# Kernel optimization log

Hardware: AMD Instinct MI355X
Metric: run time of the kernel (lower is better)

The kernel has to match this reference:

```python
import jax, jax.numpy as jnp
import numpy as np
import math

B, T, H = 2, 1024, 2048
NH, NKV, HD = 8, 2, 256
S = 4           # altup_num_inputs
FF = 8192       # intermediate_size
LR = 64         # laurel_rank
EPS = 1e-6
ROPE_THETA = 1e6


def _ln(x, w):
    # Gemma3nRMSNorm in this repo: fp32 mean-subtract then F.layer_norm (no bias)
    x32 = x.astype(jnp.float32)
    xc = x32 - x32.mean(-1, keepdims=True)
    var = (xc * xc).mean(-1, keepdims=True)
    return (xc * jax.lax.rsqrt(var + EPS) * w.astype(jnp.float32)).astype(x.dtype)


def _rotate_half(x):
    x1, x2 = jnp.split(x, 2, axis=-1)
    return jnp.concatenate((-x2, x1), axis=-1)


def _rope(x, cos, sin):  # x: [B,nh,T,hd]; cos/sin: [B,T,hd]
    return x * cos[:, None] + _rotate_half(x) * sin[:, None]


def setup_inputs() -> dict:
    key = jax.random.key(0)
    ks = jax.random.split(key, 24)

    def w(k, shape, scale=0.02):
        return jax.random.normal(k, shape, jnp.float32) * scale

    hidden_states = jax.random.normal(ks[0], (S, B, T, H), jnp.float32)

    # real rotary embeddings
    inv_freq = 1.0 / (ROPE_THETA ** (np.arange(0, HD, 2, dtype=np.float64) / HD))
    freqs = np.arange(T, dtype=np.float64)[:, None] * inv_freq[None, :]
    emb = np.concatenate([freqs, freqs], axis=-1)  # [T,HD]
    cos = jnp.broadcast_to(jnp.asarray(np.cos(emb), jnp.float32)[None], (B, T, HD))
    sin = jnp.broadcast_to(jnp.asarray(np.sin(emb), jnp.float32)[None], (B, T, HD))

    return {
        "hidden_states": hidden_states, "cos": cos, "sin": sin,
        "wq": w(ks[1], (NH * HD, H)), "wk": w(ks[2], (NKV * HD, H)),
        "wv": w(ks[3], (NKV * HD, H)), "wo": w(ks[4], (H, NH * HD)),
        "q_norm_w": jnp.ones((HD,), jnp.float32), "k_norm_w": jnp.ones((HD,), jnp.float32),
        "input_ln_w": jnp.ones((H,), jnp.float32), "post_attn_ln_w": jnp.ones((H,), jnp.float32),
        "pre_ffw_ln_w": jnp.ones((H,), jnp.float32), "post_ffw_ln_w": jnp.ones((H,), jnp.float32),
        "gate_w": w(ks[5], (FF, H)), "up_w": w(ks[6], (FF, H)), "down_w": w(ks[7], (H, FF)),
        "laurel_left_w": w(ks[8], (LR, H)), "laurel_right_w": w(ks[9], (H, LR)),
        "laurel_norm_w": jnp.ones((H,), jnp.float32),
        "router_norm_w": jnp.ones((H,), jnp.float32),
        "router_w": w(ks[10], (S, H)),
        "pred_coef_w": w(ks[11], (S * S, S)),
        "corr_coef_w": w(ks[12], (S, S)),
        "correct_output_scale": w(ks[13], (H,), 1.0),
    }


def reference(hidden_states, cos, sin, wq, wk, wv, wo, q_norm_w, k_norm_w,
              input_ln_w, post_attn_ln_w, pre_ffw_ln_w, post_ffw_ln_w,
              gate_w, up_w, down_w, laurel_left_w, laurel_right_w, laurel_norm_w,
              router_norm_w, router_w, pred_coef_w, corr_coef_w, correct_output_scale):
    def modalities_of(x):  # router: RMSNorm -> scale -> linear -> tanh
        r = _ln(x, router_norm_w) * (1.0 / H)
        return jnp.tanh((r @ router_w.T).astype(jnp.float32)).astype(x.dtype)

    # ---- AltUp predict ----
    m = modalities_of(hidden_states[0])                      # [B,T,S]
    coefs = (m @ pred_coef_w.T).reshape(B, T, S, S)          # raw [B,T,S_out,S_in]
    # torch: matmul(h.permute(1,2,3,0), coefs.permute(0,1,3,2)) => sum_s h[s]*raw[...,j,s]
    predictions = jnp.einsum('sbth,btjs->jbth', hidden_states, coefs) + hidden_states

    active = predictions[0]
    x_norm = _ln(active, input_ln_w)

    # ---- Laurel block ----
    lau = (x_norm @ laurel_left_w.T) @ laurel_right_w.T
    laurel_out = x_norm + _ln(lau, laurel_norm_w)

    # ---- Attention (GQA, q/k/v norms, rope, scale=1.0) ----
    q = _ln((x_norm @ wq.T).reshape(B, T, NH, HD), q_norm_w).transpose(0, 2, 1, 3)
    q = _rope(q, cos, sin)
    k = _ln((x_norm @ wk.T).reshape(B, T, NKV, HD), k_norm_w).transpose(0, 2, 1, 3)
    k = _rope(k, cos, sin)
    v = _ln((x_norm @ wv.T).reshape(B, T, NKV, HD), jnp.ones((HD,), jnp.float32))
    v = v.transpose(0, 2, 1, 3)
    rep = NH // NKV
    k = jnp.repeat(k, rep, axis=1)
    v = jnp.repeat(v, rep, axis=1)
    scores = jnp.einsum('bhqd,bhkd->bhqk', q, k)             # scaling = 1.0 in Gemma3n
    causal = jnp.tril(jnp.ones((T, T), bool))
    scores = jnp.where(causal, scores, jnp.finfo(jnp.float32).min)
    attn = jax.nn.softmax(scores.astype(jnp.float32), axis=-1).astype(q.dtype)
    out = jnp.einsum('bhqk,bhkd->bhqd', attn, v)
    out = out.transpose(0, 2, 1, 3).reshape(B, T, NH * HD) @ wo.T
    out = _ln(out, post_attn_ln_w)

    attn_gated = active + out
    attn_laurel = (attn_gated + laurel_out) * (1.0 / math.sqrt(2.0))

    # ---- MLP (gelu-tanh gated) ----
    h = _ln(attn_laurel, pre_ffw_ln_w)
    ffw = (jax.nn.gelu(h @ gate_w.T, approximate=True) * (h @ up_w.T)) @ down_w.T
    ffw = _ln(ffw, post_ffw_ln_w)
    activated = attn_laurel + ffw

    # ---- AltUp correct ----
    mc = modalities_of(activated)                            # [B,T,S]
    innovation = activated - predictions[0]                  # [B,T,H]
    ccoefs = (mc @ corr_coef_w.T) + 1.0                      # [B,T,S]
    corrected = innovation[None] * ccoefs.transpose(2, 0, 1)[..., None] + predictions

    # scale_corrected_output on the active stream (altup_correct_scale=True)
    first = (corrected[0] * correct_output_scale).astype(corrected.dtype)
    corrected = corrected.at[0].set(first)
    return corrected
```

## Files before the change

### kernel.cpp

```cpp
#include <hip/hip_runtime.h>
#include <hip/hip_bf16.h>
#include <math.h>

#define B_   2
#define T_   1024
#define H_   2048
#define NH_  8
#define NKV_ 2
#define HD_  256
#define S_   4
#define FF_  8192
#define LR_  64
#define ROWS_ (B_*T_)
#define EPS_ 1e-6f

typedef __attribute__((ext_vector_type(8))) __bf16 bf16x8;
typedef __attribute__((ext_vector_type(4))) float floatx4;
typedef __attribute__((ext_vector_type(8))) unsigned short ushort8v;

__device__ __forceinline__ unsigned short f2bf(float f) {
    unsigned int u = __float_as_uint(f);
    return (unsigned short)((u + 0x7FFFu + ((u >> 16) & 1u)) >> 16);
}

__device__ __forceinline__ void gl_lds16(const void* g, void* l) {
    __builtin_amdgcn_global_load_lds(
        (const __attribute__((address_space(1))) void*)g,
        (__attribute__((address_space(3))) void*)l, 16, 0, 0);
}

__device__ __forceinline__ float block_sum(float v) {
    __shared__ float s4[4];
    #pragma unroll
    for (int o = 32; o > 0; o >>= 1) v += __shfl_down(v, o, 64);
    int lane = threadIdx.x & 63;
    int w    = threadIdx.x >> 6;
    __syncthreads();
    if (lane == 0) s4[w] = v;
    __syncthreads();
    return s4[0] + s4[1] + s4[2] + s4[3];
}

__device__ __forceinline__ float block_max(float v) {
    __shared__ float s4m[4];
    #pragma unroll
    for (int o = 32; o > 0; o >>= 1) v = fmaxf(v, __shfl_down(v, o, 64));
    int lane = threadIdx.x & 63;
    int w    = threadIdx.x >> 6;
    __syncthreads();
    if (lane == 0) s4m[w] = v;
    __syncthreads();
    return fmaxf(fmaxf(s4m[0], s4m[1]), fmaxf(s4m[2], s4m[3]));
}

__global__ __launch_bounds__(256) void cvt_bf16(
    const float* __restrict__ in, unsigned short* __restrict__ out, int n)
{
    int i = (blockIdx.x * 256 + threadIdx.x) * 8;
    if (i >= n) return;
    float4 v0 = *reinterpret_cast<const float4*>(in + i);
    float4 v1 = *reinterpret_cast<const float4*>(in + i + 4);
    ushort8v o;
    o[0] = f2bf(v0.x); o[1] = f2bf(v0.y); o[2] = f2bf(v0.z); o[3] = f2bf(v0.w);
    o[4] = f2bf(v1.x); o[5] = f2bf(v1.y); o[6] = f2bf(v1.z); o[7] = f2bf(v1.w);
    *reinterpret_cast<ushort8v*>(out + i) = o;
}

__global__ __launch_bounds__(256) void router_kernel(
    const float* __restrict__ x, const float* __restrict__ nw,
    const float* __restrict__ rw, float* __restrict__ mout)
{
    size_t row = blockIdx.x;
    int tid = threadIdx.x;
    const float* xr = x + row * H_;
    float v[8]; float s = 0.f;
    #pragma unroll
    for (int i = 0; i < 8; ++i) { v[i] = xr[i*256 + tid]; s += v[i]; }
    float mu = block_sum(s) * (1.f / H_);
    float ss = 0.f;
    #pragma unroll
    for (int i = 0; i < 8; ++i) { float c = v[i] - mu; ss += c * c; }
    float rstd = rsqrtf(block_sum(ss) * (1.f / H_) + EPS_);
    float n[8];
    #pragma unroll
    for (int i = 0; i < 8; ++i) n[i] = (v[i] - mu) * rstd * nw[i*256 + tid];
    for (int so = 0; so < S_; ++so) {
        float p = 0.f;
        #pragma unroll
        for (int i = 0; i < 8; ++i) p += n[i] * rw[(size_t)so * H_ + i*256 + tid];
        float dot = block_sum(p);
        if (tid == 0) mout[row * S_ + so] = tanhf(dot * (1.f / H_));
    }
}

__global__ __launch_bounds__(256) void predict_kernel(
    const float* __restrict__ hid, const float* __restrict__ m,
    const float* __restrict__ pcw, float* __restrict__ pred)
{
    size_t row = blockIdx.x;
    int tid = threadIdx.x;
    __shared__ float ms[4];
    __shared__ float c[16];
    if (tid < 4) ms[tid] = m[row * S_ + tid];
    __syncthreads();
    if (tid < 16) {
        float s = 0.f;
        #pragma unroll
        for (int i = 0; i < 4; ++i) s += ms[i] * pcw[tid * 4 + i];
        c[tid] = s;
    }
    __syncthreads();
    const size_t STRIDE = (size_t)ROWS_ * H_;
    #pragma unroll
    for (int i = 0; i < 8; ++i) {
        size_t idx = row * H_ + i*256 + tid;
        float h0 = hid[idx];
        float h1 = hid[idx + STRIDE];
        float h2 = hid[idx + 2*STRIDE];
        float h3 = hid[idx + 3*STRIDE];
        float hv[4] = {h0, h1, h2, h3};
        #pragma unroll
        for (int j = 0; j < 4; ++j) {
            float val = hv[j] + h0*c[j*4+0] + h1*c[j*4+1] + h2*c[j*4+2] + h3*c[j*4+3];
            pred[idx + (size_t)j * STRIDE] = val;
        }
    }
}

__global__ __launch_bounds__(256) void ln_residual(
    const float* __restrict__ x, const float* __restrict__ xadd,
    const float* __restrict__ w,
    const float* __restrict__ a1, const float* __restrict__ a2,
    float scale, float* __restrict__ out, unsigned short* __restrict__ outb)
{
    size_t row = blockIdx.x;
    int tid = threadIdx.x;
    const float* xr = x + row * H_;
    const float* xa = xadd ? xadd + row * H_ : nullptr;
    float v[8]; float s = 0.f;
    #pragma unroll
    for (int i = 0; i < 8; ++i) {
        v[i] = xr[i*256 + tid];
        if (xa) v[i] += xa[i*256 + tid];
        s += v[i];
    }
    float mu = block_sum(s) * (1.f / H_);
    float ss = 0.f;
    #pragma unroll
    for (int i = 0; i < 8; ++i) { float c = v[i] - mu; ss += c * c; }
    float rstd = rsqrtf(block_sum(ss) * (1.f / H_) + EPS_);
    #pragma unroll
    for (int i = 0; i < 8; ++i) {
        size_t idx = row * H_ + i*256 + tid;
        float y = (v[i] - mu) * rstd * w[i*256 + tid];
        if (a1) y += a1[idx];
        if (a2) y += a2[idx];
        y *= scale;
        if (out)  out[idx]  = y;
        if (outb) outb[idx] = f2bf(y);
    }
}

#define BM 64
#define BN 64
#define BK 32
#define LDP 68

__global__ __launch_bounds__(256) void gemm_nt(
    const float* __restrict__ A, const float* __restrict__ Bm,
    float* __restrict__ C, int M, int N, int K)
{
    __shared__ float As[BK][LDP];
    __shared__ float Bs[BK][LDP];
    int tid = threadIdx.x;
    int n0 = blockIdx.x * BN;
    int m0 = blockIdx.y * BM;
    int tx = tid & 15, ty = tid >> 4;
    int lrow = tid >> 3;
    int lk   = (tid & 7) << 2;
    float acc[4][4] = {};
    for (int k0 = 0; k0 < K; k0 += BK) {
        #pragma unroll
        for (int r = 0; r < 2; ++r) {
            int row = lrow + r * 32;
            float4 a4 = *reinterpret_cast<const float4*>(&A[(size_t)(m0 + row) * K + k0 + lk]);
            As[lk+0][row] = a4.x; As[lk+1][row] = a4.y; As[lk+2][row] = a4.z; As[lk+3][row] = a4.w;
            float4 b4 = *reinterpret_cast<const float4*>(&Bm[(size_t)(n0 + row) * K + k0 + lk]);
            Bs[lk+0][row] = b4.x; Bs[lk+1][row] = b4.y; Bs[lk+2][row] = b4.z; Bs[lk+3][row] = b4.w;
        }
        __syncthreads();
        #pragma unroll
        for (int k = 0; k < BK; ++k) {
            float4 av = *reinterpret_cast<const float4*>(&As[k][ty << 2]);
            float4 bv = *reinterpret_cast<const float4*>(&Bs[k][tx << 2]);
            float a[4] = {av.x, av.y, av.z, av.w};
            float b[4] = {bv.x, bv.y, bv.z, bv.w};
            #pragma unroll
            for (int i = 0; i < 4; ++i)
                #pragma unroll
                for (int j = 0; j < 4; ++j)
                    acc[i][j] = fmaf(a[i], b[j], acc[i][j]);
        }
        __syncthreads();
    }
    #pragma unroll
    for (int i = 0; i < 4; ++i) {
        float4 o; o.x = acc[i][0]; o.y = acc[i][1]; o.z = acc[i][2]; o.w = acc[i][3];
        *reinterpret_cast<float4*>(&C[(size_t)(m0 + (ty << 2) + i) * N + n0 + (tx << 2)]) = o;
    }
}

__global__ __launch_bounds__(256) void gemm_bf16nt(
    const unsigned short* __restrict__ A, const unsigned short* __restrict__ Bm,
    float* __restrict__ C, float* __restrict__ C2, int M, int N, int K)
{
    __shared__ unsigned short As[4096];
    __shared__ unsigned short Bs[4096];
    int tid = threadIdx.x;
    int lane = tid & 63;
    int wave = tid >> 6;
    int m0 = blockIdx.y * 128, n0 = blockIdx.x * 128;
    int Kper = K / gridDim.z;
    int kbeg = blockIdx.z * Kper;
    int kend = kbeg + Kper;
    int wm = (wave >> 1) * 64;
    int wn = (wave & 1) * 64;
    floatx4 acc[4][4] = {};

    const unsigned short* aG0 = A  + (size_t)(m0 + lane)      * K + wave * 8;
    const unsigned short* aG1 = A  + (size_t)(m0 + 64 + lane) * K + wave * 8;
    const unsigned short* bG0 = Bm + (size_t)(n0 + lane)      * K + wave * 8;
    const unsigned short* bG1 = Bm + (size_t)(n0 + 64 + lane) * K + wave * 8;
    unsigned short* aL0 = &As[wave * 1024];
    unsigned short* aL1 = &As[wave * 1024 + 512];
    unsigned short* bL0 = &Bs[wave * 1024];
    unsigned short* bL1 = &Bs[wave * 1024 + 512];

    int kc = lane >> 4, mr = lane & 15;
    for (int k0 = kbeg; k0 < kend; k0 += 32) {
        __syncthreads();
        gl_lds16(aG0 + k0, aL0);
        gl_lds16(aG1 + k0, aL1);
        gl_lds16(bG0 + k0, bL0);
        gl_lds16(bG1 + k0, bL1);
        __syncthreads();
        bf16x8 af[4], bfv[4];
        #pragma unroll
        for (int mi = 0; mi < 4; ++mi)
            af[mi] = *reinterpret_cast<const bf16x8*>(&As[kc * 1024 + (wm + mi * 16 + mr) * 8]);
        #pragma unroll
        for (int ni = 0; ni < 4; ++ni)
            bfv[ni] = *reinterpret_cast<const bf16x8*>(&Bs[kc * 1024 + (wn + ni * 16 + mr) * 8]);
        #pragma unroll
        for (int mi = 0; mi < 4; ++mi)
            #pragma unroll
            for (int ni = 0; ni < 4; ++ni)
                acc[mi][ni] = __builtin_amdgcn_mfma_f32_16x16x32_bf16(af[mi], bfv[ni], acc[mi][ni], 0, 0, 0);
    }
    float* Cout = (blockIdx.z == 0) ? C : C2;
    int quad = lane >> 4;
    #pragma unroll
    for (int mi = 0; mi < 4; ++mi)
        #pragma unroll
        for (int ni = 0; ni < 4; ++ni)
            #pragma unroll
            for (int r = 0; r < 4; ++r)
                Cout[(size_t)(m0 + wm + mi * 16 + quad * 4 + r) * N + n0 + wn + ni * 16 + mr] = acc[mi][ni][r];
}

__global__ __launch_bounds__(256) void gemm_gateup_bf16(
    const unsigned short* __restrict__ A, const unsigned short* __restrict__ G,
    const unsigned short* __restrict__ U, unsigned short* __restrict__ Cbf,
    int M, int N, int K)
{
    __shared__ unsigned short As[4096];
    __shared__ unsigned short Gs[2048];
    __shared__ unsigned short Us[2048];
    int tid = threadIdx.x;
    int lane = tid & 63;
    int wave = tid >> 6;
    int m0 = blockIdx.y * 128, n0 = blockIdx.x * 64;
    floatx4 accg[2][4] = {};
    floatx4 accu[2][4] = {};

    const unsigned short* aG0 = A + (size_t)(m0 + lane)      * K + wave * 8;
    const unsigned short* aG1 = A + (size_t)(m0 + 64 + lane) * K + wave * 8;
    const unsigned short* gG  = G + (size_t)(n0 + lane)      * K + wave * 8;
    const unsigned short* uG  = U + (size_t)(n0 + lane)      * K + wave * 8;
    unsigned short* aL0 = &As[wave * 1024];
    unsigned short* aL1 = &As[wave * 1024 + 512];
    unsigned short* gL  = &Gs[wave * 512];
    unsigned short* uL  = &Us[wave * 512];

    int kc = lane >> 4, mr = lane & 15;
    for (int k0 = 0; k0 < K; k0 += 32) {
        __syncthreads();
        gl_lds16(aG0 + k0, aL0);
        gl_lds16(aG1 + k0, aL1);
        gl_lds16(gG + k0, gL);
        gl_lds16(uG + k0, uL);
        __syncthreads();
        bf16x8 af[2], gf[4], uf[4];
        #pragma unroll
        for (int mi = 0; mi < 2; ++mi)
            af[mi] = *reinterpret_cast<const bf16x8*>(&As[kc * 1024 + (wave * 32 + mi * 16 + mr) * 8]);
        #pragma unroll
        for (int ni = 0; ni < 4; ++ni) {
            gf[ni] = *reinterpret_cast<const bf16x8*>(&Gs[kc * 512 + (ni * 16 + mr) * 8]);
            uf[ni] = *reinterpret_cast<const bf16x8*>(&Us[kc * 512 + (ni * 16 + mr) * 8]);
        }
        #pragma unroll
        for (int mi = 0; mi < 2; ++mi)
            #pragma unroll
            for (int ni = 0; ni < 4; ++ni) {
                accg[mi][ni] = __builtin_amdgcn_mfma_f32_16x16x32_bf16(af[mi], gf[ni], accg[mi][ni], 0, 0, 0);
                accu[mi][ni] = __builtin_amdgcn_mfma_f32_16x16x32_bf16(af[mi], uf[ni], accu[mi][ni], 0, 0, 0);
            }
    }
    int quad = lane >> 4;
    #pragma unroll
    for (int mi = 0; mi < 2; ++mi) {
        int rb = m0 + wave * 32 + mi * 16 + quad * 4;
        #pragma unroll
        for (int ni = 0; ni < 4; ++ni)
            #pragma unroll
            for (int r = 0; r < 4; ++r) {
                float g = accg[mi][ni][r];
                float gl = 0.5f * g * (1.f + tanhf(0.7978845608028654f * (g + 0.044715f * g * g * g)));
                float val = gl * accu[mi][ni][r];
                Cbf[(size_t)(rb + r) * N + n0 + ni * 16 + mr] = f2bf(val);
            }
    }
}

__global__ __launch_bounds__(256) void qkv_norm_rope_fused(
    const float* __restrict__ in, const float* __restrict__ qw,
    const float* __restrict__ kw,
    const float* __restrict__ cs, const float* __restrict__ sn,
    unsigned short* __restrict__ qo, unsigned short* __restrict__ ko,
    unsigned short* __restrict__ vo)
{
    int blk = blockIdx.x;
    int hh = blk % 12;
    int trow = blk / 12;
    int b = trow / T_;
    int t = trow % T_;
    int d = threadIdx.x;
    float x = in[(size_t)trow * 3072 + hh * HD_ + d];
    float mu = block_sum(x) * (1.f / HD_);
    float xc = x - mu;
    float var = block_sum(xc * xc) * (1.f / HD_);
    float wv_ = (hh < 8) ? qw[d] : (hh < 10 ? kw[d] : 1.f);
    float n = xc * rsqrtf(var + EPS_) * wv_;
    __shared__ float buf[HD_];
    buf[d] = n;
    __syncthreads();
    float val = n;
    if (hh < 10) {
        float c = cs[(size_t)trow * HD_ + d];
        float s = sn[(size_t)trow * HD_ + d];
        float other = (d < 128) ? -buf[d + 128] : buf[d - 128];
        val = n * c + other * s;
    }
    if (hh < 8)
        qo[(((size_t)b * NH_ + hh) * T_ + t) * HD_ + d] = f2bf(val);
    else if (hh < 10)
        ko[(((size_t)b * NKV_ + (hh - 8)) * T_ + t) * HD_ + d] = f2bf(val);
    else
        vo[(((size_t)b * NKV_ + (hh - 10)) * HD_ + d) * T_ + t] = f2bf(val);
}

__global__ __launch_bounds__(256) void qk_gemm(
    const unsigned short* __restrict__ Q, const unsigned short* __restrict__ Kt,
    float* __restrict__ S, int head_base)
{
    if (blockIdx.x > blockIdx.y) return;
    int z = blockIdx.z;
    int bh = head_base + z;
    const unsigned short* A  = Q  + (size_t)bh * T_ * HD_;
    const unsigned short* Bm = Kt + (size_t)(bh >> 2) * T_ * HD_;
    float* C = S + (size_t)z * T_ * T_;

    __shared__ unsigned short As[4096];
    __shared__ unsigned short Bs[4096];
    int tid = threadIdx.x;
    int lane = tid & 63;
    int wave = tid >> 6;
    int m0 = blockIdx.y * 128, n0 = blockIdx.x * 128;
    int wm = (wave >> 1) * 64;
    int wn = (wave & 1) * 64;
    floatx4 acc[4][4] = {};

    const unsigned short* aG0 = A  + (size_t)(m0 + lane)      * HD_ + wave * 8;
    const unsigned short* aG1 = A  + (size_t)(m0 + 64 + lane) * HD_ + wave * 8;
    const unsigned short* bG0 = Bm + (size_t)(n0 + lane)      * HD_ + wave * 8;
    const unsigned short* bG1 = Bm + (size_t)(n0 + 64 + lane) * HD_ + wave * 8;
    unsigned short* aL0 = &As[wave * 1024];
    unsigned short* aL1 = &As[wave * 1024 + 512];
    unsigned short* bL0 = &Bs[wave * 1024];
    unsigned short* bL1 = &Bs[wave * 1024 + 512];

    int kc = lane >> 4, mr = lane & 15;
    for (int k0 = 0; k0 < HD_; k0 += 32) {
        __syncthreads();
        gl_lds16(aG0 + k0, aL0);
        gl_lds16(aG1 + k0, aL1);
        gl_lds16(bG0 + k0, bL0);
        gl_lds16(bG1 + k0, bL1);
        __syncthreads();
        bf16x8 af[4], bfv[4];
        #pragma unroll
        for (int mi = 0; mi < 4; ++mi)
            af[mi] = *reinterpret_cast<const bf16x8*>(&As[kc * 1024 + (wm + mi * 16 + mr) * 8]);
        #pragma unroll
        for (int ni = 0; ni < 4; ++ni)
            bfv[ni] = *reinterpret_cast<const bf16x8*>(&Bs[kc * 1024 + (wn + ni * 16 + mr) * 8]);
        #pragma unroll
        for (int mi = 0; mi < 4; ++mi)
            #pragma unroll
            for (int ni = 0; ni < 4; ++ni)
                acc[mi][ni] = __builtin_amdgcn_mfma_f32_16x16x32_bf16(af[mi], bfv[ni], acc[mi][ni], 0, 0, 0);
    }
    int quad = lane >> 4;
    #pragma unroll
    for (int mi = 0; mi < 4; ++mi)
        #pragma unroll
        for (int ni = 0; ni < 4; ++ni)
            #pragma unroll
            for (int r = 0; r < 4; ++r)
                C[(size_t)(m0 + wm + mi * 16 + quad * 4 + r) * T_ + n0 + wn + ni * 16 + mr] = acc[mi][ni][r];
}

__global__ __launch_bounds__(256) void softmax_causal(
    const float* __restrict__ S, unsigned short* __restrict__ P)
{
    int qi = blockIdx.x;
    int g  = blockIdx.y;
    int tid = threadIdx.x;
    int L = qi + 1;
    const float* Srow = S + ((size_t)g * T_ + qi) * T_;
    unsigned short* Prow = P + ((size_t)g * T_ + qi) * T_;
    float v[4];
    float mx = -3.402823466e38f;
    #pragma unroll
    for (int i = 0; i < 4; ++i) {
        int idx = i * 256 + tid;
        v[i] = (idx < L) ? Srow[idx] : -3.402823466e38f;
        mx = fmaxf(mx, v[i]);
    }
    mx = block_max(mx);
    float sm = 0.f;
    float e[4];
    #pragma unroll
    for (int i = 0; i < 4; ++i) {
        int idx = i * 256 + tid;
        e[i] = (idx < L) ? expf(v[i] - mx) : 0.f;
        sm += e[i];
    }
    sm = block_sum(sm);
    float inv = 1.f / sm;
    #pragma unroll
    for (int i = 0; i < 4; ++i)
        Prow[i * 256 + tid] = f2bf(e[i] * inv);
}

__global__ __launch_bounds__(256) void pv_gemm(
    const unsigned short* __restrict__ P, const unsigned short* __restrict__ Vt,
    unsigned short* __restrict__ Out)
{
    int z = blockIdx.z;
    int b = z >> 3;
    int h = z & 7;
    const unsigned short* A  = P  + (size_t)z * T_ * T_;
    const unsigned short* Bm = Vt + (size_t)(z >> 2) * HD_ * T_;

    __shared__ unsigned short As[4096];
    __shared__ unsigned short Bs[4096];
    int tid = threadIdx.x;
    int lane = tid & 63;
    int wave = tid >> 6;
    int m0 = blockIdx.y * 128, n0 = blockIdx.x * 128;
    int Kend = m0 + 128;
    int wm = (wave >> 1) * 64;
    int wn = (wave & 1) * 64;
    floatx4 acc[4][4] = {};

    const unsigned short* aG0 = A  + (size_t)(m0 + lane)      * T_ + wave * 8;
    const unsigned short* aG1 = A  + (size_t)(m0 + 64 + lane) * T_ + wave * 8;
    const unsigned short* bG0 = Bm + (size_t)(n0 + lane)      * T_ + wave * 8;
    const unsigned short* bG1 = Bm + (size_t)(n0 + 64 + lane) * T_ + wave * 8;
    unsigned short* aL0 = &As[wave * 1024];
    unsigned short* aL1 = &As[wave * 1024 + 512];
    unsigned short* bL0 = &Bs[wave * 1024];
    unsigned short* bL1 = &Bs[wave * 1024 + 512];

    int kc = lane >> 4, mr = lane & 15;
    for (int k0 = 0; k0 < Kend; k0 += 32) {
        __syncthreads();
        gl_lds16(aG0 + k0, aL0);
        gl_lds16(aG1 + k0, aL1);
        gl_lds16(bG0 + k0, bL0);
        gl_lds16(bG1 + k0, bL1);
        __syncthreads();
        bf16x8 af[4], bfv[4];
        #pragma unroll
        for (int mi = 0; mi < 4; ++mi)
            af[mi] = *reinterpret_cast<const bf16x8*>(&As[kc * 1024 + (wm + mi * 16 + mr) * 8]);
        #pragma unroll
        for (int ni = 0; ni < 4; ++ni)
            bfv[ni] = *reinterpret_cast<const bf16x8*>(&Bs[kc * 1024 + (wn + ni * 16 + mr) * 8]);
        #pragma unroll
        for (int mi = 0; mi < 4; ++mi)
            #pragma unroll
            for (int ni = 0; ni < 4; ++ni)
                acc[mi][ni] = __builtin_amdgcn_mfma_f32_16x16x32_bf16(af[mi], bfv[ni], acc[mi][ni], 0, 0, 0);
    }
    int quad = lane >> 4;
    #pragma unroll
    for (int mi = 0; mi < 4; ++mi)
        #pragma unroll
        for (int ni = 0; ni < 4; ++ni)
            #pragma unroll
            for (int r = 0; r < 4; ++r) {
                int row = m0 + wm + mi * 16 + quad * 4 + r;
                int col = n0 + wn + ni * 16 + mr;
                Out[((size_t)(b * T_ + row)) * (NH_ * HD_) + h * HD_ + col] =
                    f2bf(acc[mi][ni][r]);
            }
}

__global__ __launch_bounds__(256) void correct_kernel(
    const float* __restrict__ act, const float* __restrict__ pred,
    const float* __restrict__ mc, const float* __restrict__ ccw,
    const float* __restrict__ cscale, float* __restrict__ out)
{
    size_t row = blockIdx.x;
    int tid = threadIdx.x;
    __shared__ float ms[4];
    __shared__ float cc[4];
    if (tid < 4) ms[tid] = mc[row * S_ + tid];
    __syncthreads();
    if (tid < 4) {
        float s = 1.f;
        #pragma unroll
        for (int i = 0; i < 4; ++i) s += ms[i] * ccw[tid * 4 + i];
        cc[tid] = s;
    }
    __syncthreads();
    const size_t STRIDE = (size_t)ROWS_ * H_;
    #pragma unroll
    for (int i = 0; i < 8; ++i) {
        size_t idx = row * H_ + i*256 + tid;
        float a  = act[idx];
        float p0 = pred[idx];
        float inn = a - p0;
        #pragma unroll
        for (int j = 0; j < 4; ++j) {
            float val = inn * cc[j] + pred[idx + (size_t)j * STRIDE];
            if (j == 0) val *= cscale[i*256 + tid];
            out[idx + (size_t)j * STRIDE] = val;
        }
    }
}

extern "C" void kernel_launch(void* const* d_in, const int* in_sizes, int n_in,
                              void* d_out, int out_size, void* d_ws, size_t ws_size,
                              hipStream_t stream)
{
    (void)in_sizes; (void)n_in; (void)out_size; (void)ws_size;
    const float* hidden         = (const float*)d_in[0];
    const float* cosp           = (const float*)d_in[1];
    const float* sinp           = (const float*)d_in[2];
    const float* wq             = (const float*)d_in[3];
    const float* wk             = (const float*)d_in[4];
    const float* wv             = (const float*)d_in[5];
    const float* wo             = (const float*)d_in[6];
    const float* q_norm_w       = (const float*)d_in[7];
    const float* k_norm_w       = (const float*)d_in[8];
    const float* input_ln_w     = (const float*)d_in[9];
    const float* post_attn_ln_w = (const float*)d_in[10];
    const float* pre_ffw_ln_w   = (const float*)d_in[11];
    const float* post_ffw_ln_w  = (const float*)d_in[12];
    const float* gate_w         = (const float*)d_in[13];
    const float* up_w           = (const float*)d_in[14];
    const float* down_w         = (const float*)d_in[15];
    const float* ll_w           = (const float*)d_in[16];
    const float* lr_w           = (const float*)d_in[17];
    const float* laurel_norm_w  = (const float*)d_in[18];
    const float* router_norm_w  = (const float*)d_in[19];
    const float* router_w       = (const float*)d_in[20];
    const float* pred_coef_w    = (const float*)d_in[21];
    const float* corr_coef_w    = (const float*)d_in[22];
    const float* cscale         = (const float*)d_in[23];
    float* outp = (float*)d_out;

    char* base = (char*)d_ws;
    float* pred   = (float*)base;              base += 67108864;
    float* xnorm  = (float*)base;              base += 16777216;
    unsigned short* xnorm_bf = (unsigned short*)base; base += 8388608;
    float* lout   = (float*)base;              base += 16777216;
    float* alaur  = (float*)base;              base += 16777216;
    float* tmpH   = (float*)base;              base += 16777216;
    float* mbuf   = (float*)base;              base += 32768;
    float* mcbuf  = (float*)base;              base += 32768;
    float* ltmp   = (float*)base;              base += 524288;
    char* arena = base;
    unsigned short* qkvw_bf = (unsigned short*)arena;
    float* qkv_pre = (float*)(arena + 12582912);
    unsigned short* Pbuf    = (unsigned short*)arena;
    unsigned short* q_bf    = (unsigned short*)(arena + 37748736);
    unsigned short* k_bf    = (unsigned short*)(arena + 46137344);
    unsigned short* vT_bf   = (unsigned short*)(arena + 48234496);
    unsigned short* attn_bf = (unsigned short*)(arena + 50331648);
    unsigned short* wo_bf   = (unsigned short*)(arena + 58720256);
    float* Sbuf             = (float*)(arena + 67108864);
    unsigned short* gate_bf = (unsigned short*)arena;
    unsigned short* up_bf   = (unsigned short*)(arena + 33554432);
    unsigned short* gu_bf   = (unsigned short*)(arena + 67108864);
    unsigned short* down_bf = gate_bf;
    float* activated = lout;

    router_kernel <<<ROWS_, 256, 0, stream>>>(hidden, router_norm_w, router_w, mbuf);
    predict_kernel<<<ROWS_, 256, 0, stream>>>(hidden, mbuf, pred_coef_w, pred);
    ln_residual   <<<ROWS_, 256, 0, stream>>>(pred, nullptr, input_ln_w, nullptr, nullptr, 1.f, xnorm, xnorm_bf);

    gemm_nt<<<dim3(LR_/BN, ROWS_/BM), 256, 0, stream>>>(xnorm, ll_w, ltmp, ROWS_, LR_, H_);
    gemm_nt<<<dim3(H_/BN,  ROWS_/BM), 256, 0, stream>>>(ltmp, lr_w, tmpH, ROWS_, H_, LR_);
    ln_residual<<<ROWS_, 256, 0, stream>>>(tmpH, nullptr, laurel_norm_w, xnorm, nullptr, 1.f, lout, nullptr);

    cvt_bf16<<<2048, 256, 0, stream>>>(wq, qkvw_bf,            4194304);
    cvt_bf16<<< 512, 256, 0, stream>>>(wk, qkvw_bf + 4194304,  1048576);
    cvt_bf16<<< 512, 256, 0, stream>>>(wv, qkvw_bf + 5242880,  1048576);
    gemm_bf16nt<<<dim3(24, 16, 1), 256, 0, stream>>>(xnorm_bf, qkvw_bf, qkv_pre, nullptr, ROWS_, 3072, H_);
    qkv_norm_rope_fused<<<ROWS_*12, 256, 0, stream>>>(qkv_pre, q_norm_w, k_norm_w, cosp, sinp, q_bf, k_bf, vT_bf);
    cvt_bf16<<<2048, 256, 0, stream>>>(wo, wo_bf, 4194304);
    for (int hb = 0; hb < B_ * NH_; hb += 8) {
        qk_gemm       <<<dim3(8, 8, 8), 256, 0, stream>>>(q_bf, k_bf, Sbuf, hb);
        softmax_causal<<<dim3(T_, 8),   256, 0, stream>>>(Sbuf, Pbuf + (size_t)hb * T_ * T_);
    }
    pv_gemm<<<dim3(2, 8, 16), 256, 0, stream>>>(Pbuf, vT_bf, attn_bf);
    gemm_bf16nt<<<dim3(16, 16, 2), 256, 0, stream>>>(attn_bf, wo_bf, tmpH, xnorm, ROWS_, H_, NH_*HD_);
    ln_residual<<<ROWS_, 256, 0, stream>>>(tmpH, xnorm, post_attn_ln_w, pred, lout, 0.7071067811865475f, alaur, nullptr);

    ln_residual<<<ROWS_, 256, 0, stream>>>(alaur, nullptr, pre_ffw_ln_w, nullptr, nullptr, 1.f, nullptr, xnorm_bf);
    cvt_bf16<<<8192, 256, 0, stream>>>(gate_w, gate_bf, 16777216);
    cvt_bf16<<<8192, 256, 0, stream>>>(up_w,   up_bf,   16777216);
    gemm_gateup_bf16<<<dim3(128, 16), 256, 0, stream>>>(xnorm_bf, gate_bf, up_bf, gu_bf, ROWS_, FF_, H_);
    cvt_bf16<<<8192, 256, 0, stream>>>(down_w, down_bf, 16777216);
    gemm_bf16nt<<<dim3(16, 16, 2), 256, 0, stream>>>(gu_bf, down_bf, tmpH, xnorm, ROWS_, H_, FF_);
    ln_residual<<<ROWS_, 256, 0, stream>>>(tmpH, xnorm, post_ffw_ln_w, alaur, nullptr, 1.f, activated, nullptr);

    router_kernel <<<ROWS_, 256, 0, stream>>>(activated, router_norm_w, router_w, mcbuf);
    correct_kernel<<<ROWS_, 256, 0, stream>>>(activated, pred, mcbuf, corr_coef_w, cscale, outp);
}
```

Before: 1.202 ms.

## Double-buffer LDS tiles in the MFMA GEMM kernels to overlap loads with compute

New measurement: 1.183 ms. No clear change (-1.6%).

```diff
diff --git a/kernel.cpp b/kernel.cpp
--- a/kernel.cpp
+++ b/kernel.cpp
@@ -214,8 +214,8 @@
     const unsigned short* __restrict__ A, const unsigned short* __restrict__ Bm,
     float* __restrict__ C, float* __restrict__ C2, int M, int N, int K)
 {
-    __shared__ unsigned short As[4096];
-    __shared__ unsigned short Bs[4096];
+    __shared__ unsigned short As[8192];
+    __shared__ unsigned short Bs[8192];
     int tid = threadIdx.x;
     int lane = tid & 63;
     int wave = tid >> 6;
@@ -231,31 +231,44 @@
     const unsigned short* aG1 = A  + (size_t)(m0 + 64 + lane) * K + wave * 8;
     const unsigned short* bG0 = Bm + (size_t)(n0 + lane)      * K + wave * 8;
     const unsigned short* bG1 = Bm + (size_t)(n0 + 64 + lane) * K + wave * 8;
-    unsigned short* aL0 = &As[wave * 1024];
-    unsigned short* aL1 = &As[wave * 1024 + 512];
-    unsigned short* bL0 = &Bs[wave * 1024];
-    unsigned short* bL1 = &Bs[wave * 1024 + 512];
 
     int kc = lane >> 4, mr = lane & 15;
+
+    {
+        unsigned short* a = &As[wave * 1024];
+        unsigned short* b = &Bs[wave * 1024];
+        gl_lds16(aG0 + kbeg, a);
+        gl_lds16(aG1 + kbeg, a + 512);
+        gl_lds16(bG0 + kbeg, b);
+        gl_lds16(bG1 + kbeg, b + 512);
+    }
+    __syncthreads();
+    int cur = 0;
     for (int k0 = kbeg; k0 < kend; k0 += 32) {
-        __syncthreads();
-        gl_lds16(aG0 + k0, aL0);
-        gl_lds16(aG1 + k0, aL1);
-        gl_lds16(bG0 + k0, bL0);
-        gl_lds16(bG1 + k0, bL1);
-        __syncthreads();
+        if (k0 + 32 < kend) {
+            int nb = (cur ^ 1) * 4096;
+            unsigned short* a = &As[nb + wave * 1024];
+            unsigned short* b = &Bs[nb + wave * 1024];
+            gl_lds16(aG0 + k0 + 32, a);
+            gl_lds16(aG1 + k0 + 32, a + 512);
+            gl_lds16(bG0 + k0 + 32, b);
+            gl_lds16(bG1 + k0 + 32, b + 512);
+        }
+        int cb = cur * 4096;
         bf16x8 af[4], bfv[4];
         #pragma unroll
         for (int mi = 0; mi < 4; ++mi)
-            af[mi] = *reinterpret_cast<const bf16x8*>(&As[kc * 1024 + (wm + mi * 16 + mr) * 8]);
+            af[mi] = *reinterpret_cast<const bf16x8*>(&As[cb + kc * 1024 + (wm + mi * 16 + mr) * 8]);
         #pragma unroll
         for (int ni = 0; ni < 4; ++ni)
-            bfv[ni] = *reinterpret_cast<const bf16x8*>(&Bs[kc * 1024 + (wn + ni * 16 + mr) * 8]);
+            bfv[ni] = *reinterpret_cast<const bf16x8*>(&Bs[cb + kc * 1024 + (wn + ni * 16 + mr) * 8]);
         #pragma unroll
         for (int mi = 0; mi < 4; ++mi)
             #pragma unroll
             for (int ni = 0; ni < 4; ++ni)
                 acc[mi][ni] = __builtin_amdgcn_mfma_f32_16x16x32_bf16(af[mi], bfv[ni], acc[mi][ni], 0, 0, 0);
+        __syncthreads();
+        cur ^= 1;
     }
     float* Cout = (blockIdx.z == 0) ? C : C2;
     int quad = lane >> 4;
@@ -273,9 +286,9 @@
     const unsigned short* __restrict__ U, unsigned short* __restrict__ Cbf,
     int M, int N, int K)
 {
-    __shared__ unsigned short As[4096];
-    __shared__ unsigned short Gs[2048];
-    __shared__ unsigned short Us[2048];
+    __shared__ unsigned short As[8192];
+    __shared__ unsigned short Gs[4096];
+    __shared__ unsigned short Us[4096];
     int tid = threadIdx.x;
     int lane = tid & 63;
     int wave = tid >> 6;
@@ -287,27 +300,35 @@
     const unsigned short* aG1 = A + (size_t)(m0 + 64 + lane) * K + wave * 8;
     const unsigned short* gG  = G + (size_t)(n0 + lane)      * K + wave * 8;
     const unsigned short* uG  = U + (size_t)(n0 + lane)      * K + wave * 8;
-    unsigned short* aL0 = &As[wave * 1024];
-    unsigned short* aL1 = &As[wave * 1024 + 512];
-    unsigned short* gL  = &Gs[wave * 512];
-    unsigned short* uL  = &Us[wave * 512];
 
     int kc = lane >> 4, mr = lane & 15;
+
+    {
+        gl_lds16(aG0, &As[wave * 1024]);
+        gl_lds16(aG1, &As[wave * 1024 + 512]);
+        gl_lds16(gG,  &Gs[wave * 512]);
+        gl_lds16(uG,  &Us[wave * 512]);
+    }
+    __syncthreads();
+    int cur = 0;
     for (int k0 = 0; k0 < K; k0 += 32) {
-        __syncthreads();
-        gl_lds16(aG0 + k0, aL0);
-        gl_lds16(aG1 + k0, aL1);
-        gl_lds16(gG + k0, gL);
-        gl_lds16(uG + k0, uL);
-        __syncthreads();
+        if (k0 + 32 < K) {
+            int a_nb = (cur ^ 1) * 4096;
+            int g_nb = (cur ^ 1) * 2048;
+            gl_lds16(aG0 + k0 + 32, &As[a_nb + wave * 1024]);
+            gl_lds16(aG1 + k0 + 32, &As[a_nb + wave * 1024 + 512]);
+            gl_lds16(gG + k0 + 32,  &Gs[g_nb + wave * 512]);
+            gl_lds16(uG + k0 + 32,  &Us[g_nb + wave * 512]);
+        }
+        int ab = cur * 4096, gb = cur * 2048;
         bf16x8 af[2], gf[4], uf[4];
         #pragma unroll
         for (int mi = 0; mi < 2; ++mi)
-            af[mi] = *reinterpret_cast<const bf16x8*>(&As[kc * 1024 + (wave * 32 + mi * 16 + mr) * 8]);
+            af[mi] = *reinterpret_cast<const bf16x8*>(&As[ab + kc * 1024 + (wave * 32 + mi * 16 + mr) * 8]);
         #pragma unroll
         for (int ni = 0; ni < 4; ++ni) {
-            gf[ni] = *reinterpret_cast<const bf16x8*>(&Gs[kc * 512 + (ni * 16 + mr) * 8]);
-            uf[ni] = *reinterpret_cast<const bf16x8*>(&Us[kc * 512 + (ni * 16 + mr) * 8]);
+            gf[ni] = *reinterpret_cast<const bf16x8*>(&Gs[gb + kc * 512 + (ni * 16 + mr) * 8]);
+            uf[ni] = *reinterpret_cast<const bf16x8*>(&Us[gb + kc * 512 + (ni * 16 + mr) * 8]);
         }
         #pragma unroll
         for (int mi = 0; mi < 2; ++mi)
@@ -316,6 +337,8 @@
                 accg[mi][ni] = __builtin_amdgcn_mfma_f32_16x16x32_bf16(af[mi], gf[ni], accg[mi][ni], 0, 0, 0);
                 accu[mi][ni] = __builtin_amdgcn_mfma_f32_16x16x32_bf16(af[mi], uf[ni], accu[mi][ni], 0, 0, 0);
             }
+        __syncthreads();
+        cur ^= 1;
     }
     int quad = lane >> 4;
     #pragma unroll
@@ -381,8 +404,8 @@
     const unsigned short* Bm = Kt + (size_t)(bh >> 2) * T_ * HD_;
     float* C = S + (size_t)z * T_ * T_;
 
-    __shared__ unsigned short As[4096];
-    __shared__ unsigned short Bs[4096];
+    __shared__ unsigned short As[8192];
+    __shared__ unsigned short Bs[8192];
     int tid = threadIdx.x;
     int lane = tid & 63;
     int wave = tid >> 6;
@@ -395,31 +418,40 @@
     const unsigned short* aG1 = A  + (size_t)(m0 + 64 + lane) * HD_ + wave * 8;
     const unsigned short* bG0 = Bm + (size_t)(n0 + lane)      * HD_ + wave * 8;
     const unsigned short* bG1 = Bm + (size_t)(n0 + 64 + lane) * HD_ + wave * 8;
-    unsigned short* aL0 = &As[wave * 1024];
-    unsigned short* aL1 = &As[wave * 1024 + 512];
-    unsigned short* bL0 = &Bs[wave * 1024];
-    unsigned short* bL1 = &Bs[wave * 1024 + 512];
 
     int kc = lane >> 4, mr = lane & 15;
+
+    {
+        gl_lds16(aG0, &As[wave * 1024]);
+        gl_lds16(aG1, &As[wave * 1024 + 512]);
+        gl_lds16(bG0, &Bs[wave * 1024]);
+        gl_lds16(bG1, &Bs[wave * 1024 + 512]);
+    }
+    __syncthreads();
+    int cur = 0;
     for (int k0 = 0; k0 < HD_; k0 += 32) {
-        __syncthreads();
-        gl_lds16(aG0 + k0, aL0);
-        gl_lds16(aG1 + k0, aL1);
-        gl_lds16(bG0 + k0, bL0);
-        gl_lds16(bG1 + k0, bL1);
-        __syncthreads();
+        if (k0 + 32 < HD_) {
+            int nb = (cur ^ 1) * 4096;
+            gl_lds16(aG0 + k0 + 32, &As[nb + wave * 1024]);
+            gl_lds16(aG1 + k0 + 32, &As[nb + wave * 1024 + 512]);
+            gl_lds16(bG0 + k0 + 32, &Bs[nb + wave * 1024]);
+            gl_lds16(bG1 + k0 + 32, &Bs[nb + wave * 1024 + 512]);
+        }
+        int cb = cur * 4096;
         bf16x8 af[4], bfv[4];
         #pragma unroll
         for (int mi = 0; mi < 4; ++mi)
-            af[mi] = *reinterpret_cast<const bf16x8*>(&As[kc * 1024 + (wm + mi * 16 + mr) * 8]);
+            af[mi] = *reinterpret_cast<const bf16x8*>(&As[cb + kc * 1024 + (wm + mi * 16 + mr) * 8]);
         #pragma unroll
         for (int ni = 0; ni < 4; ++ni)
-            bfv[ni] = *reinterpret_cast<const bf16x8*>(&Bs[kc * 1024 + (wn + ni * 16 + mr) * 8]);
+            bfv[ni] = *reinterpret_cast<const bf16x8*>(&Bs[cb + kc * 1024 + (wn + ni * 16 + mr) * 8]);
         #pragma unroll
         for (int mi = 0; mi < 4; ++mi)
             #pragma unroll
             for (int ni = 0; ni < 4; ++ni)
                 acc[mi][ni] = __builtin_amdgcn_mfma_f32_16x16x32_bf16(af[mi], bfv[ni], acc[mi][ni], 0, 0, 0);
+        __syncthreads();
+        cur ^= 1;
     }
     int quad = lane >> 4;
     #pragma unroll
@@ -474,8 +506,8 @@
     const unsigned short* A  = P  + (size_t)z * T_ * T_;
     const unsigned short* Bm = Vt + (size_t)(z >> 2) * HD_ * T_;
 
-    __shared__ unsigned short As[4096];
-    __shared__ unsigned short Bs[4096];
+    __shared__ unsigned short As[8192];
+    __shared__ unsigned short Bs[8192];
     int tid = threadIdx.x;
     int lane = tid & 63;
     int wave = tid >> 6;
@@ -489,31 +521,40 @@
     const unsigned short* aG1 = A  + (size_t)(m0 + 64 + lane) * T_ + wave * 8;
     const unsigned short* bG0 = Bm + (size_t)(n0 + lane)      * T_ + wave * 8;
     const unsigned short* bG1 = Bm + (size_t)(n0 + 64 + lane) * T_ + wave * 8;
-    unsigned short* aL0 = &As[wave * 1024];
-    unsigned short* aL1 = &As[wave * 1024 + 512];
-    unsigned short* bL0 = &Bs[wave * 1024];
-    unsigned short* bL1 = &Bs[wave * 1024 + 512];
 
     int kc = lane >> 4, mr = lane & 15;
+
+    {
+        gl_lds16(aG0, &As[wave * 1024]);
+        gl_lds16(aG1, &As[wave * 1024 + 512]);
+        gl_lds16(bG0, &Bs[wave * 1024]);
+        gl_lds16(bG1, &Bs[wave * 1024 + 512]);
+    }
+    __syncthreads();
+    int cur = 0;
     for (int k0 = 0; k0 < Kend; k0 += 32) {
-        __syncthreads();
-        gl_lds16(aG0 + k0, aL0);
-        gl_lds16(aG1 + k0, aL1);
-        gl_lds16(bG0 + k0, bL0);
-        gl_lds16(bG1 + k0, bL1);
-        __syncthreads();
+        if (k0 + 32 < Kend) {
+            int nb = (cur ^ 1) * 4096;
+            gl_lds16(aG0 + k0 + 32, &As[nb + wave * 1024]);
+            gl_lds16(aG1 + k0 + 32, &As[nb + wave * 1024 + 512]);
+            gl_lds16(bG0 + k0 + 32, &Bs[nb + wave * 1024]);
+            gl_lds16(bG1 + k0 + 32, &Bs[nb + wave * 1024 + 512]);
+        }
+        int cb = cur * 4096;
         bf16x8 af[4], bfv[4];
         #pragma unroll
         for (int mi = 0; mi < 4; ++mi)
-            af[mi] = *reinterpret_cast<const bf16x8*>(&As[kc * 1024 + (wm + mi * 16 + mr) * 8]);
+            af[mi] = *reinterpret_cast<const bf16x8*>(&As[cb + kc * 1024 + (wm + mi * 16 + mr) * 8]);
         #pragma unroll
         for (int ni = 0; ni < 4; ++ni)
-            bfv[ni] = *reinterpret_cast<const bf16x8*>(&Bs[kc * 1024 + (wn + ni * 16 + mr) * 8]);
+            bfv[ni] = *reinterpret_cast<const bf16x8*>(&Bs[cb + kc * 1024 + (wn + ni * 16 + mr) * 8]);
         #pragma unroll
         for (int mi = 0; mi < 4; ++mi)
             #pragma unroll
             for (int ni = 0; ni < 4; ++ni)
                 acc[mi][ni] = __builtin_amdgcn_mfma_f32_16x16x32_bf16(af[mi], bfv[ni], acc[mi][ni], 0, 0, 0);
+        __syncthreads();
+        cur ^= 1;
     }
     int quad = lane >> 4;
     #pragma unroll
```
